# Kernel tuning notes

Hardware: AMD Instinct MI355X
Metric: run time of the kernel (lower is better)

## Reference

```python
import jax, jax.numpy as jnp
import numpy as np

B, T = 256, 25
PRE = 2048   # resnet feature dim
D = 256      # fc_early_dim = cell_size = in_size = hybrid_in_size
K = 4        # num_atts
NC = 2       # num_classes


def setup_inputs() -> dict:
    key = jax.random.key(0)
    ks = jax.random.split(key, 20)
    def p(k, *s):
        return jax.random.normal(k, s, jnp.float32) * 0.02
    z = lambda *s: jnp.zeros(s, jnp.float32)
    return {
        "x_visual": jax.random.normal(ks[0], (B, T, PRE), jnp.float32),
        "x_tactile": jax.random.normal(ks[1], (B, T, PRE), jnp.float32),
        "fc0_w": p(ks[2], PRE, D), "fc0_b": z(D),
        "fc1_w": p(ks[3], PRE, D), "fc1_b": z(D),
        # LSTHM_V: W(x) + U(h) + V(z), gates packed as [f,i,o,ch]
        "lv_W": p(ks[4], D, 4 * D), "lv_U": p(ks[5], D, 4 * D), "lv_V": p(ks[6], D, 4 * D), "lv_b": z(4 * D),
        # LSTHM_T
        "lt_W": p(ks[7], D, 4 * D), "lt_U": p(ks[8], D, 4 * D), "lt_V": p(ks[9], D, 4 * D), "lt_b": z(4 * D),
        # MAB: attention over concat hidden (2D) producing K attentions
        "att_w": p(ks[10], 2 * D, K * 2 * D), "att_b": z(K * 2 * D),
        "red_v_w": p(ks[11], K * D, D), "red_v_b": z(D),
        "red_t_w": p(ks[12], K * D, D), "red_t_b": z(D),
        "mab_out_w": p(ks[13], 2 * D, D), "mab_out_b": z(D),
        "late0_w": p(ks[14], 2 * D, D), "late0_b": z(D),
        "late1_w": p(ks[15], D, NC), "late1_b": z(NC),
    }


def _lsthm(x, c, h, zz, W, U, V, b):
    s = x @ W + h @ U + zz @ V + b            # [B, 4D]
    f = jax.nn.sigmoid(s[:, :D])
    i = jax.nn.sigmoid(s[:, D:2 * D])
    o = jax.nn.sigmoid(s[:, 2 * D:3 * D])
    ch = jnp.tanh(s[:, 3 * D:])
    c_new = f * c + i * ch
    return c_new, jnp.tanh(c_new) * o


def reference(x_visual, x_tactile, fc0_w, fc0_b, fc1_w, fc1_b,
              lv_W, lv_U, lv_V, lv_b, lt_W, lt_U, lt_V, lt_b,
              att_w, att_b, red_v_w, red_v_b, red_t_w, red_t_b,
              mab_out_w, mab_out_b, late0_w, late0_b, late1_w, late1_b):
    xv = x_visual @ fc0_w + fc0_b             # [B, T, D]
    xt = x_tactile @ fc1_w + fc1_b            # [B, T, D]

    def mab(h_v, h_t):
        h = jnp.concatenate([h_v, h_t], -1)   # [B, 2D]
        att = jax.nn.softmax(h @ att_w + att_b, axis=-1)       # [B, K*2D]
        attd = att.reshape(-1, K, 2 * D) * h[:, None, :]        # K attended copies
        v = attd[:, :, :D].reshape(-1, K * D)
        t = attd[:, :, D:].reshape(-1, K * D)
        rv = jax.nn.relu(v @ red_v_w + red_v_b)
        rt = jax.nn.relu(t @ red_t_w + red_t_b)
        return jnp.concatenate([rv, rt], -1) @ mab_out_w + mab_out_b  # [B, D]

    def step(carry, xs):
        c_v, h_v, c_t, h_t, zz = carry
        xvi, xti = xs
        c_v, h_v = _lsthm(xvi, c_v, h_v, zz, lv_W, lv_U, lv_V, lv_b)
        c_t, h_t = _lsthm(xti, c_t, h_t, zz, lt_W, lt_U, lt_V, lt_b)
        zz = mab(h_v, h_t)
        return (c_v, h_v, c_t, h_t, zz), None

    zeros = jnp.zeros((x_visual.shape[0], D), jnp.float32)
    init = (zeros, zeros, zeros, zeros, zeros)
    (c_v, h_v, c_t, h_t, zz), _ = jax.lax.scan(
        step, init, (jnp.swapaxes(xv, 0, 1), jnp.swapaxes(xt, 0, 1)))
    x = jnp.concatenate([h_v, h_t], -1) @ late0_w + late0_b
    return x @ late1_w + late1_b              # dropout is identity in eval
```

## Files before the change

### kernel.cpp

```cpp
#include <hip/hip_runtime.h>

typedef unsigned short u16;
typedef unsigned int u32;
typedef unsigned long long u64;
using bfrag = __attribute__((ext_vector_type(8))) short;
using facc  = __attribute__((ext_vector_type(4))) float;

#define DEV __device__ __forceinline__
#define AGT __HIP_MEMORY_SCOPE_AGENT

static constexpr size_t o_xv   = 0;
static constexpr size_t o_xt   = 3276800;
static constexpr size_t o_f0T  = 6553600;
static constexpr size_t o_f1T  = 7602176;
static constexpr size_t o_UVWv = 8650752;
static constexpr size_t o_UVWt = 10747904;
static constexpr size_t o_attT = 12845056;
static constexpr size_t o_redT = 14942208;
static constexpr size_t o_bgv  = 15990784;
static constexpr size_t o_bgt  = 15994880;
static constexpr size_t o_mvv  = 15998976;
static constexpr size_t o_mvt  = 16003072;
static constexpr size_t o_FW   = 16007168;
static constexpr size_t o_fb   = 16011264;
static constexpr size_t o_eh   = 16011520;
static constexpr size_t o_psum = 41177344;
static constexpr size_t o_hv   = 42750208;
static constexpr size_t o_ht   = 46158080;
static constexpr size_t o_rvt  = 49565952;
static constexpr size_t o_bar  = 56119552;
static constexpr size_t o_end  = 56120576;

DEV u16 f2bf(float f) {
    u32 u = __float_as_uint(f);
    u32 r = (u + 0x7FFFu + ((u >> 16) & 1u)) >> 16;
    return (u16)r;
}
DEV float bf2f(u16 h) { return __uint_as_float(((u32)h) << 16); }
DEV u32 pk2(float a, float b) { return (u32)f2bf(a) | ((u32)f2bf(b) << 16); }
DEV float sigm(float x) { return 1.0f / (1.0f + __expf(-x)); }
DEV float tanh2(float x) { return 2.0f * sigm(2.0f * x) - 1.0f; }
DEV facc mfma16(bfrag a, bfrag b, facc c) {
    return __builtin_amdgcn_mfma_f32_16x16x32_bf16(a, b, c, 0, 0, 0);
}

DEV void gbar(u32* bar, int bid, u32 k) {
    asm volatile("s_waitcnt vmcnt(0)" ::: "memory");
    __syncthreads();
    if (threadIdx.x == 0) {
        __builtin_amdgcn_fence(__ATOMIC_RELEASE, "agent");
        u32 old = __hip_atomic_fetch_add(&bar[(bid & 7) * 16], 1u, __ATOMIC_RELAXED, AGT);
        if (old == k * 32u - 1u)
            __hip_atomic_fetch_add(&bar[128], 1u, __ATOMIC_RELAXED, AGT);
        while (__hip_atomic_load(&bar[128], __ATOMIC_RELAXED, AGT) < k * 8u)
            __builtin_amdgcn_s_sleep(2);
    }
    __syncthreads();
}


DEV void prep_T(const float* __restrict__ src, u16* dst, int lgK, int N, int nb, int bl, int tid) {
    int pairs = ((1 << lgK) * N) >> 1;
    int kmask = (1 << lgK) - 1;
    for (int idx = bl * 256 + tid; idx < pairs; idx += nb * 256) {
        int i = idx * 2;
        int n = i >> lgK, k = i & kmask;
        *(u32*)&dst[i] = pk2(src[(size_t)k * N + n], src[(size_t)(k + 1) * N + n]);
    }
}

DEV void prep_UVW(const float* U, const float* mo, const float* V, const float* W,
                  u16* dst, int nb, int bl, int tid) {
    for (int idx = bl * 256 + tid; idx < 1024 * 1024; idx += nb * 256) {
        int p = idx >> 10, k = idx & 1023;
        int j = p >> 2, g = p & 3, gc = g * 256 + j;
        float v;
        if (k < 256) v = U[(size_t)k * 1024 + gc];
        else if (k < 768) {
            int s = k - 256;
            float a = 0.f;
            for (int d = 0; d < 256; ++d) a += mo[s * 256 + d] * V[(size_t)d * 1024 + gc];
            v = a;
        } else v = W[(size_t)(k - 768) * 1024 + gc];
        dst[idx] = f2bf(v);
    }
}

DEV void prep_bias(const float* lb, const float* mob, const float* V,
                   float* bg, float* mv, int nb, int bl, int tid) {
    for (int p = bl * 256 + tid; p < 1024; p += nb * 256) {
        int j = p >> 2, g = p & 3, gc = g * 256 + j;
        bg[p] = lb[gc];
        float a = 0.f;
        for (int d = 0; d < 256; ++d) a += mob[d] * V[(size_t)d * 1024 + gc];
        mv[p] = a;
    }
}

DEV void prep_FW(const float* l0w, const float* l0b, const float* l1w, const float* l1b,
                 float* FW, float* fb, int tid) {
    for (int idx = tid; idx < 1024; idx += 256) {
        int k = idx >> 1, c = idx & 1;
        float a = 0.f;
        for (int j = 0; j < 256; ++j) a += l0w[k * 256 + j] * l1w[j * 2 + c];
        FW[idx] = a;
    }
    if (tid < 2) {
        float a = l1b[tid];
        for (int j = 0; j < 256; ++j) a += l0b[j] * l1w[j * 2 + tid];
        fb[tid] = a;
    }
}

struct KP { const float* in[26]; char* ws; float* out; };

__global__ __launch_bounds__(256) void marn_all(KP P) {
    __shared__ __align__(16) unsigned char SM[31744];
    int tid = threadIdx.x, b = blockIdx.x;
    int w = tid >> 6, l = tid & 63, lm = l & 15, kh = l >> 4;
    u32 bk = 0;
    char* ws = P.ws;

    u16* xv = (u16*)(ws + o_xv);
    u16* xt = (u16*)(ws + o_xt);
    u16* f0T = (u16*)(ws + o_f0T);
    u16* f1T = (u16*)(ws + o_f1T);
    u16* UVWv = (u16*)(ws + o_UVWv);
    u16* UVWt = (u16*)(ws + o_UVWt);
    u16* attT = (u16*)(ws + o_attT);
    u16* redT = (u16*)(ws + o_redT);
    float* bgv = (float*)(ws + o_bgv);
    float* bgt = (float*)(ws + o_bgt);
    float* mvv = (float*)(ws + o_mvv);
    float* mvt = (float*)(ws + o_mvt);
    float* FW = (float*)(ws + o_FW);
    float* fb = (float*)(ws + o_fb);
    u16* ehB = (u16*)(ws + o_eh);
    float* psB = (float*)(ws + o_psum);
    u16* hvB = (u16*)(ws + o_hv);
    u16* htB = (u16*)(ws + o_ht);
    u16* rvB = (u16*)(ws + o_rvt);
    u32* bar = (u32*)(ws + o_bar);
    const float* attb = P.in[15];
    const float* rvb = P.in[17];
    const float* rtb = P.in[19];

    if      (b < 24)  prep_T(P.in[2], f0T, 11, 256, 24, b, tid);
    else if (b < 48)  prep_T(P.in[4], f1T, 11, 256, 24, b - 24, tid);
    else if (b < 96)  prep_T(P.in[14], attT, 9, 2048, 48, b - 48, tid);
    else if (b < 108) prep_T(P.in[16], redT, 10, 256, 12, b - 96, tid);
    else if (b < 120) prep_T(P.in[18], redT + 256 * 1024, 10, 256, 12, b - 108, tid);
    else if (b < 176) prep_UVW(P.in[7], P.in[20], P.in[8], P.in[6], UVWv, 56, b - 120, tid);
    else if (b < 232) prep_UVW(P.in[11], P.in[20], P.in[12], P.in[10], UVWt, 56, b - 176, tid);
    else if (b < 236) prep_bias(P.in[9], P.in[21], P.in[8], bgv, mvv, 4, b - 232, tid);
    else if (b < 240) prep_bias(P.in[13], P.in[21], P.in[12], bgt, mvt, 4, b - 236, tid);
    else if (b == 240) prep_FW(P.in[22], P.in[23], P.in[24], P.in[25], FW, fb, tid);
    gbar(bar, b, ++bk);

    {
        u16* Al = (u16*)SM;
        u16* Bl = (u16*)(SM + 9216);
        u16* Lt = (u16*)SM;
        for (int u = b; u < 400; u += 256) {
            int zs = u & 1, ny = (u >> 1) & 1, mx = u >> 2;
            const float* A = zs ? P.in[1] : P.in[0];
            const u16* BT = zs ? f1T : f0T;
            const float* bias = zs ? P.in[5] : P.in[3];
            u16* C = zs ? xt : xv;
            int m0 = mx * 64, n0 = ny * 128;
            int arow = tid >> 2, aseg = tid & 3;
            int brow = tid >> 1, bseg = tid & 1;
            facc acc[8];
#pragma unroll
            for (int i = 0; i < 8; ++i) acc[i] = (facc){0.f, 0.f, 0.f, 0.f};
            for (int c = 0; c < 32; ++c) {
                float4 av[4];
#pragma unroll
                for (int uu = 0; uu < 4; ++uu)
                    av[uu] = *(const float4*)&A[(size_t)(m0 + arow) * 2048 + c * 64 + aseg * 16 + uu * 4];
                uint4 bv[4];
#pragma unroll
                for (int uu = 0; uu < 4; ++uu)
                    bv[uu] = *(const uint4*)&BT[(size_t)(n0 + brow) * 2048 + c * 64 + bseg * 32 + uu * 8];
                __syncthreads();
                u32 pk[8];
#pragma unroll
                for (int uu = 0; uu < 4; ++uu) {
                    pk[2 * uu] = pk2(av[uu].x, av[uu].y);
                    pk[2 * uu + 1] = pk2(av[uu].z, av[uu].w);
                }
                *(uint4*)&Al[arow * 72 + aseg * 16] = make_uint4(pk[0], pk[1], pk[2], pk[3]);
                *(uint4*)&Al[arow * 72 + aseg * 16 + 8] = make_uint4(pk[4], pk[5], pk[6], pk[7]);
#pragma unroll
                for (int uu = 0; uu < 4; ++uu)
                    *(uint4*)&Bl[brow * 72 + bseg * 32 + uu * 8] = bv[uu];
                __syncthreads();
#pragma unroll
                for (int ks = 0; ks < 2; ++ks) {
                    bfrag a = *(const bfrag*)&Al[(16 * w + lm) * 72 + ks * 32 + kh * 8];
#pragma unroll
                    for (int tt = 0; tt < 8; ++tt) {
                        bfrag bb = *(const bfrag*)&Bl[(tt * 16 + lm) * 72 + ks * 32 + kh * 8];
                        acc[tt] = mfma16(a, bb, acc[tt]);
                    }
                }
            }
            __syncthreads();
#pragma unroll
            for (int tt = 0; tt < 8; ++tt)
#pragma unroll
                for (int j = 0; j < 4; ++j)
                    Lt[(16 * w + 4 * kh + j) * 128 + tt * 16 + lm] = f2bf(acc[tt][j] + bias[n0 + tt * 16 + lm]);
            __syncthreads();
            {
                int mloc = tid >> 2, seg = tid & 3;
                int mg = m0 + mloc;
                int bi = mg / 25, ti = mg - bi * 25;
                u16* drow = &C[(size_t)(ti * 256 + bi) * 256 + n0 + seg * 32];
                const uint4* lp = (const uint4*)&Lt[mloc * 128 + seg * 32];
#pragma unroll
                for (int i = 0; i < 4; ++i)
                    *(uint4*)&drow[i * 8] = lp[i];
            }
            __syncthreads();
        }
    }
    gbar(bar, b, ++bk);

    float* sscr = (float*)SM;
    float* ppart = (float*)(SM + 26112);
    float* sinvl = (float*)(SM + 27136);
    float* redscr = (float*)(SM + 27200);
    float creg[2] = {0.f, 0.f};

    for (int t = 0; t < 25; ++t) {
        const u16* hv_t = hvB + t * 65536;
        const u16* ht_t = htB + t * 65536;
        u16* hv_n = hvB + (t + 1) * 65536;
        u16* ht_n = htB + (t + 1) * 65536;
        const u16* rv_t = rvB + t * 131072;

        {
            int m = b & 3, n = b >> 2;
            int r0 = m * 64;
            bool sv = (n < 32);
            int p0 = (sv ? n : n - 32) * 32;
            const u16* UVW = sv ? UVWv : UVWt;
            const u16* hb = sv ? hv_t : ht_t;
            const u16* xb = (sv ? xv : xt) + t * 65536;
            int arow = r0 + 16 * w + lm;
            const u16* Ah = hb + arow * 256 + kh * 8;
            const u16* Ar = rv_t + arow * 512 + kh * 8;
            const u16* Ax = xb + arow * 256 + kh * 8;
            const u16* B0 = UVW + (size_t)(p0 + lm) * 1024 + kh * 8;
            const u16* B1 = UVW + (size_t)(p0 + 16 + lm) * 1024 + kh * 8;
            facc acc0 = (facc){0.f, 0.f, 0.f, 0.f}, acc1 = (facc){0.f, 0.f, 0.f, 0.f};
#pragma unroll
            for (int ks = 0; ks < 8; ++ks) {
                bfrag a = *(const bfrag*)(Ah + ks * 32);
                bfrag b0 = *(const bfrag*)(B0 + ks * 32);
                bfrag b1 = *(const bfrag*)(B1 + ks * 32);
                acc0 = mfma16(a, b0, acc0);
                acc1 = mfma16(a, b1, acc1);
            }
#pragma unroll
            for (int ks = 0; ks < 16; ++ks) {
                bfrag a = *(const bfrag*)(Ar + ks * 32);
                bfrag b0 = *(const bfrag*)(B0 + 256 + ks * 32);
                bfrag b1 = *(const bfrag*)(B1 + 256 + ks * 32);
                acc0 = mfma16(a, b0, acc0);
                acc1 = mfma16(a, b1, acc1);
            }
#pragma unroll
            for (int ks = 0; ks < 8; ++ks) {
                bfrag a = *(const bfrag*)(Ax + ks * 32);
                bfrag b0 = *(const bfrag*)(B0 + 768 + ks * 32);
                bfrag b1 = *(const bfrag*)(B1 + 768 + ks * 32);
                acc0 = mfma16(a, b0, acc0);
                acc1 = mfma16(a, b1, acc1);
            }
            __syncthreads();
#pragma unroll
            for (int j = 0; j < 4; ++j) {
                sscr[(16 * w + 4 * kh + j) * 33 + lm] = acc0[j];
                sscr[(16 * w + 4 * kh + j) * 33 + 16 + lm] = acc1[j];
            }
            __syncthreads();
            const float* bg = sv ? bgv : bgt;
            const float* mv = sv ? mvv : mvt;
            float tf = (t > 0) ? 1.0f : 0.0f;
            int r = tid >> 2, jp = tid & 3;
            float h2[2];
#pragma unroll
            for (int e = 0; e < 2; ++e) {
                int p = jp * 8 + e * 4;
                float4 b4 = *(const float4*)&bg[p0 + p];
                float4 m4 = *(const float4*)&mv[p0 + p];
                float s0 = sscr[r * 33 + p + 0] + b4.x + tf * m4.x;
                float s1 = sscr[r * 33 + p + 1] + b4.y + tf * m4.y;
                float s2 = sscr[r * 33 + p + 2] + b4.z + tf * m4.z;
                float s3 = sscr[r * 33 + p + 3] + b4.w + tf * m4.w;
                float fg = sigm(s0), ig = sigm(s1), og = sigm(s2), ch = tanh2(s3);
                float cn = fg * creg[e] + ig * ch;
                creg[e] = cn;
                h2[e] = tanh2(cn) * og;
            }
            u16* hw = sv ? hv_n : ht_n;
            *(u32*)&hw[(r0 + r) * 256 + (p0 >> 2) + jp * 2] = pk2(h2[0], h2[1]);
        }
        gbar(bar, b, ++bk);

        if (t < 24) {
            u16* eh_t = ehB + (size_t)t * 524288;
            float* ps_t = psB + t * 16384;

            {
                int m = b & 3, n = b >> 2;
                int r0 = m * 64, c0 = n * 32;
                int arow = r0 + 16 * w + lm;
                const u16* A0 = hv_n + arow * 256 + kh * 8;
                const u16* A1 = ht_n + arow * 256 + kh * 8;
                const u16* B0 = attT + (size_t)(c0 + lm) * 512 + kh * 8;
                const u16* B1 = attT + (size_t)(c0 + 16 + lm) * 512 + kh * 8;
                facc acc0 = (facc){0.f, 0.f, 0.f, 0.f}, acc1 = (facc){0.f, 0.f, 0.f, 0.f};
#pragma unroll
                for (int ks = 0; ks < 8; ++ks) {
                    bfrag a = *(const bfrag*)(A0 + ks * 32);
                    bfrag b0 = *(const bfrag*)(B0 + ks * 32);
                    bfrag b1 = *(const bfrag*)(B1 + ks * 32);
                    acc0 = mfma16(a, b0, acc0);
                    acc1 = mfma16(a, b1, acc1);
                }
#pragma unroll
                for (int ks = 0; ks < 8; ++ks) {
                    bfrag a = *(const bfrag*)(A1 + ks * 32);
                    bfrag b0 = *(const bfrag*)(B0 + 256 + ks * 32);
                    bfrag b1 = *(const bfrag*)(B1 + 256 + ks * 32);
                    acc0 = mfma16(a, b0, acc0);
                    acc1 = mfma16(a, b1, acc1);
                }
                __syncthreads();
#pragma unroll
                for (int j = 0; j < 4; ++j) {
                    sscr[(16 * w + 4 * kh + j) * 33 + lm] = acc0[j];
                    sscr[(16 * w + 4 * kh + j) * 33 + 16 + lm] = acc1[j];
                }
                __syncthreads();
                int r = tid >> 2, q = tid & 3;
                int n15 = n & 15;
                const u16* hfs = (n15 < 8) ? hv_n : ht_n;
                int hc0 = (32 * n15) & 255;
                uint4 hfv = *(const uint4*)&hfs[(r0 + r) * 256 + hc0 + q * 8];
                const u16* hfp = (const u16*)&hfv;
                float ps = 0.f;
                u32 pk[4];
#pragma unroll
                for (int x = 0; x < 4; ++x) {
                    float e0 = __expf(sscr[r * 33 + q * 8 + 2 * x] + attb[c0 + q * 8 + 2 * x]);
                    float e1 = __expf(sscr[r * 33 + q * 8 + 2 * x + 1] + attb[c0 + q * 8 + 2 * x + 1]);
                    ps += e0 + e1;
                    pk[x] = (u32)f2bf(e0 * bf2f(hfp[2 * x])) | ((u32)f2bf(e1 * bf2f(hfp[2 * x + 1])) << 16);
                }
                *(uint4*)&eh_t[(size_t)(r0 + r) * 2048 + c0 + q * 8] = make_uint4(pk[0], pk[1], pk[2], pk[3]);
                ppart[r * 4 + q] = ps;
                __syncthreads();
                if (tid < 64)
                    ps_t[n * 256 + r0 + tid] =
                        ppart[tid * 4] + ppart[tid * 4 + 1] + ppart[tid * 4 + 2] + ppart[tid * 4 + 3];
            }
            gbar(bar, b, ++bk);

            {
                int m = b & 15, n = b >> 4;
                int r0 = m * 16, nc0 = n * 32;
                int half = (n < 8) ? 0 : 1;
                if (tid < 64) {
                    int r = tid >> 2, q = tid & 3;
                    float s = 0.f;
                    for (int j2 = q * 16; j2 < q * 16 + 16; ++j2) s += ps_t[j2 * 256 + r0 + r];
                    ppart[r * 4 + q] = s;
                }
                __syncthreads();
                if (tid < 16)
                    sinvl[tid] = 1.0f / (ppart[tid * 4] + ppart[tid * 4 + 1] + ppart[tid * 4 + 2] + ppart[tid * 4 + 3]);
                int tt = w & 1, kh2 = w >> 1;
                const u16* Ab = eh_t + (size_t)(r0 + lm) * 2048 + half * 256 + kh * 8;
                const u16* Bb = redT + (size_t)(nc0 + tt * 16 + lm) * 1024 + kh * 8;
                facc acc = (facc){0.f, 0.f, 0.f, 0.f};
#pragma unroll
                for (int s = 0; s < 16; ++s) {
                    int ks = kh2 * 16 + s;
                    int kk = ks * 32;
                    int j = ((kk >> 8) << 9) + (kk & 255);
                    bfrag a = *(const bfrag*)(Ab + j);
                    bfrag bb = *(const bfrag*)(Bb + kk);
                    acc = mfma16(a, bb, acc);
                }
                __syncthreads();
                if (w >= 2) {
#pragma unroll
                    for (int j = 0; j < 4; ++j)
                        redscr[tt * 272 + (4 * kh + j) * 17 + lm] = acc[j];
                }
                __syncthreads();
                if (w < 2) {
#pragma unroll
                    for (int j = 0; j < 4; ++j) {
                        float v = acc[j] + redscr[tt * 272 + (4 * kh + j) * 17 + lm];
                        int rloc = 4 * kh + j;
                        int col = nc0 + tt * 16 + lm;
                        float bs = (col < 256) ? rvb[col] : rtb[col - 256];
                        v = fmaxf(sinvl[rloc] * v + bs, 0.0f);
                        sscr[rloc * 33 + tt * 16 + lm] = v;
                    }
                }
                __syncthreads();
                if (tid < 64) {
                    int rloc = tid >> 2, cp = tid & 3;
                    u16* rw = rvB + (size_t)(t + 1) * 131072;
                    u32 q0 = pk2(sscr[rloc * 33 + cp * 8 + 0], sscr[rloc * 33 + cp * 8 + 1]);
                    u32 q1 = pk2(sscr[rloc * 33 + cp * 8 + 2], sscr[rloc * 33 + cp * 8 + 3]);
                    u32 q2 = pk2(sscr[rloc * 33 + cp * 8 + 4], sscr[rloc * 33 + cp * 8 + 5]);
                    u32 q3 = pk2(sscr[rloc * 33 + cp * 8 + 6], sscr[rloc * 33 + cp * 8 + 7]);
                    *(uint4*)&rw[(size_t)(r0 + rloc) * 512 + nc0 + cp * 8] = make_uint4(q0, q1, q2, q3);
                }
            }
            gbar(bar, b, ++bk);
        }
    }

    {
        const u16* hv25 = hvB + 25 * 65536;
        const u16* ht25 = htB + 25 * 65536;
        if (tid < 64) {
            float a0 = 0.f, a1 = 0.f;
            u64 hv = *(const u64*)&hv25[b * 256 + tid * 4];
            u64 ht = *(const u64*)&ht25[b * 256 + tid * 4];
#pragma unroll
            for (int i = 0; i < 4; ++i) {
                int k = tid * 4 + i;
                float h0 = bf2f((u16)(hv >> (16 * i)));
                float h1 = bf2f((u16)(ht >> (16 * i)));
                a0 += h0 * FW[k * 2] + h1 * FW[(256 + k) * 2];
                a1 += h0 * FW[k * 2 + 1] + h1 * FW[(256 + k) * 2 + 1];
            }
            ppart[tid] = a0;
            ppart[64 + tid] = a1;
        }
        __syncthreads();
        if (tid < 2) {
            float s = fb[tid];
            for (int i = 0; i < 64; ++i) s += ppart[tid * 64 + i];
            P.out[b * 2 + tid] = s;
        }
    }
}


extern "C" void kernel_launch(void* const* d_in, const int* in_sizes, int n_in,
                              void* d_out, int out_size, void* d_ws, size_t ws_size,
                              hipStream_t stream) {
    (void)in_sizes; (void)n_in; (void)out_size; (void)ws_size;
    KP P;
    for (int i = 0; i < 26; ++i) P.in[i] = (const float*)d_in[i];
    P.ws = (char*)d_ws;
    P.out = (float*)d_out;

    hipMemsetAsync((char*)d_ws + o_bar, 0, 1024, stream);
    hipMemsetAsync((char*)d_ws + o_hv, 0, 131072, stream);
    hipMemsetAsync((char*)d_ws + o_ht, 0, 131072, stream);
    hipMemsetAsync((char*)d_ws + o_rvt, 0, 262144, stream);

    void* kargs[] = { &P };
    hipError_t e = hipLaunchCooperativeKernel((void*)marn_all, dim3(256), dim3(256),
                                              kargs, 0, stream);
    if (e != hipSuccess) {
        (void)hipGetLastError();
        marn_all<<<dim3(256), dim3(256), 0, stream>>>(P);
    }
}
```

Measured before the change: 1.945 ms.

## Replace counter grid barrier with per-block flag barrier and XCD-aware tile mapping

The grid barrier changes from a two-level atomic counter into per-block flags. Each block publishes its epoch with an atomic exchange, and all 256 threads each poll one peer's flag, which removes the serialized counter increments. Tile assignment is also remapped so that blocks on the same XCD (b&7) handle contiguous column groups, which should improve L2 locality of the weight slices. The trade-off is more polling traffic, and the flag region grows to 256 padded slots that are zeroed on every launch.

```diff
diff --git a/kernel.cpp b/kernel.cpp
--- a/kernel.cpp
+++ b/kernel.cpp
@@ -29,7 +29,7 @@
 static constexpr size_t o_ht   = 46158080;
 static constexpr size_t o_rvt  = 49565952;
 static constexpr size_t o_bar  = 56119552;
-static constexpr size_t o_end  = 56120576;
+static constexpr size_t o_end  = 56135936;
 
 DEV u16 f2bf(float f) {
     u32 u = __float_as_uint(f);
@@ -44,17 +44,16 @@
     return __builtin_amdgcn_mfma_f32_16x16x32_bf16(a, b, c, 0, 0, 0);
 }
 
-DEV void gbar(u32* bar, int bid, u32 k) {
+DEV void gbar(u32* flags, int b, u32 k) {
     asm volatile("s_waitcnt vmcnt(0)" ::: "memory");
     __syncthreads();
     if (threadIdx.x == 0) {
         __builtin_amdgcn_fence(__ATOMIC_RELEASE, "agent");
-        u32 old = __hip_atomic_fetch_add(&bar[(bid & 7) * 16], 1u, __ATOMIC_RELAXED, AGT);
-        if (old == k * 32u - 1u)
-            __hip_atomic_fetch_add(&bar[128], 1u, __ATOMIC_RELAXED, AGT);
-        while (__hip_atomic_load(&bar[128], __ATOMIC_RELAXED, AGT) < k * 8u)
-            __builtin_amdgcn_s_sleep(2);
-    }
+        (void)__hip_atomic_exchange(&flags[b * 16], k, __ATOMIC_RELAXED, AGT);
+    }
+    u32* myf = &flags[threadIdx.x * 16];
+    while (__hip_atomic_load(myf, __ATOMIC_RELAXED, AGT) < k)
+        __builtin_amdgcn_s_sleep(1);
     __syncthreads();
 }
 
@@ -232,6 +231,7 @@
     float* sinvl = (float*)(SM + 27136);
     float* redscr = (float*)(SM + 27200);
     float creg[2] = {0.f, 0.f};
+    int xid = b & 7, q = b >> 3;
 
     for (int t = 0; t < 25; ++t) {
         const u16* hv_t = hvB + t * 65536;
@@ -241,7 +241,7 @@
         const u16* rv_t = rvB + t * 131072;
 
         {
-            int m = b & 3, n = b >> 2;
+            int m = q & 3, n = xid * 8 + (q >> 2);
             int r0 = m * 64;
             bool sv = (n < 32);
             int p0 = (sv ? n : n - 32) * 32;
@@ -315,7 +315,7 @@
             float* ps_t = psB + t * 16384;
 
             {
-                int m = b & 3, n = b >> 2;
+                int m = q & 3, n = xid * 8 + (q >> 2);
                 int r0 = m * 64, c0 = n * 32;
                 int arow = r0 + 16 * w + lm;
                 const u16* A0 = hv_n + arow * 256 + kh * 8;
@@ -346,23 +346,23 @@
                     sscr[(16 * w + 4 * kh + j) * 33 + 16 + lm] = acc1[j];
                 }
                 __syncthreads();
-                int r = tid >> 2, q = tid & 3;
+                int r = tid >> 2, qq = tid & 3;
                 int n15 = n & 15;
                 const u16* hfs = (n15 < 8) ? hv_n : ht_n;
                 int hc0 = (32 * n15) & 255;
-                uint4 hfv = *(const uint4*)&hfs[(r0 + r) * 256 + hc0 + q * 8];
+                uint4 hfv = *(const uint4*)&hfs[(r0 + r) * 256 + hc0 + qq * 8];
                 const u16* hfp = (const u16*)&hfv;
                 float ps = 0.f;
                 u32 pk[4];
 #pragma unroll
                 for (int x = 0; x < 4; ++x) {
-                    float e0 = __expf(sscr[r * 33 + q * 8 + 2 * x] + attb[c0 + q * 8 + 2 * x]);
-                    float e1 = __expf(sscr[r * 33 + q * 8 + 2 * x + 1] + attb[c0 + q * 8 + 2 * x + 1]);
+                    float e0 = __expf(sscr[r * 33 + qq * 8 + 2 * x] + attb[c0 + qq * 8 + 2 * x]);
+                    float e1 = __expf(sscr[r * 33 + qq * 8 + 2 * x + 1] + attb[c0 + qq * 8 + 2 * x + 1]);
                     ps += e0 + e1;
                     pk[x] = (u32)f2bf(e0 * bf2f(hfp[2 * x])) | ((u32)f2bf(e1 * bf2f(hfp[2 * x + 1])) << 16);
                 }
-                *(uint4*)&eh_t[(size_t)(r0 + r) * 2048 + c0 + q * 8] = make_uint4(pk[0], pk[1], pk[2], pk[3]);
-                ppart[r * 4 + q] = ps;
+                *(uint4*)&eh_t[(size_t)(r0 + r) * 2048 + c0 + qq * 8] = make_uint4(pk[0], pk[1], pk[2], pk[3]);
+                ppart[r * 4 + qq] = ps;
                 __syncthreads();
                 if (tid < 64)
                     ps_t[n * 256 + r0 + tid] =
@@ -375,10 +375,10 @@
                 int r0 = m * 16, nc0 = n * 32;
                 int half = (n < 8) ? 0 : 1;
                 if (tid < 64) {
-                    int r = tid >> 2, q = tid & 3;
+                    int r = tid >> 2, qq = tid & 3;
                     float s = 0.f;
-                    for (int j2 = q * 16; j2 < q * 16 + 16; ++j2) s += ps_t[j2 * 256 + r0 + r];
-                    ppart[r * 4 + q] = s;
+                    for (int j2 = qq * 16; j2 < qq * 16 + 16; ++j2) s += ps_t[j2 * 256 + r0 + r];
+                    ppart[r * 4 + qq] = s;
                 }
                 __syncthreads();
                 if (tid < 16)
@@ -466,7 +466,7 @@
     P.ws = (char*)d_ws;
     P.out = (float*)d_out;
 
-    hipMemsetAsync((char*)d_ws + o_bar, 0, 1024, stream);
+    hipMemsetAsync((char*)d_ws + o_bar, 0, o_end - o_bar, stream);
     hipMemsetAsync((char*)d_ws + o_hv, 0, 131072, stream);
     hipMemsetAsync((char*)d_ws + o_ht, 0, 131072, stream);
     hipMemsetAsync((char*)d_ws + o_rvt, 0, 262144, stream);
```

Measured after the change: 1.952 ms. About the same (+0.4%).
